# Kernel optimization log

Hardware: AMD Instinct MI355X
Metric: run time of the kernel (lower is better)

Reference implementation:

```python
import jax, jax.numpy as jnp
import numpy as np
from jax import lax

B, T, D, H = 32, 2048, 512, 512


def setup_inputs() -> dict:
    key = jax.random.key(0)
    k1, k2, k3 = jax.random.split(key, 3)
    inputs = jax.random.normal(k1, (B, T, D), dtype=jnp.float32)
    input_paddings = jnp.zeros((B, T), dtype=jnp.float32)  # all tokens valid
    c0 = jnp.zeros((B, H), dtype=jnp.float32)
    h0 = jnp.zeros((B, H), dtype=jnp.float32)
    # flax LSTMCell params fused: dense_i kernel [D,4H] (no bias), dense_h kernel [H,4H] + bias [4H]
    Wi = jax.random.normal(k2, (D, 4 * H), dtype=jnp.float32) * 0.05
    Wh = jax.random.normal(k3, (H, 4 * H), dtype=jnp.float32) * 0.05
    b = jnp.zeros((4 * H,), dtype=jnp.float32)
    return {"inputs": inputs, "input_paddings": input_paddings,
            "c0": c0, "h0": h0, "Wi": Wi, "Wh": Wh, "b": b}


def reference(inputs, input_paddings, c0, h0, Wi, Wh, b):
    # reverse=False path: lengths are computed but unused.
    del input_paddings
    # Precompute input projections for all timesteps in one big GEMM: [B,T,4H]
    x_proj = jnp.einsum('btd,dg->btg', inputs, Wi)

    def step(carry, xp_t):
        c, h = carry
        z = xp_t + h @ Wh + b  # [B, 4H]
        i, f, g, o = jnp.split(z, 4, axis=-1)  # flax gate order: i, f, g, o
        c_new = jax.nn.sigmoid(f) * c + jax.nn.sigmoid(i) * jnp.tanh(g)
        h_new = jax.nn.sigmoid(o) * jnp.tanh(c_new)
        return (c_new, h_new), h_new

    xs = jnp.swapaxes(x_proj, 0, 1)  # [T, B, 4H]
    _, outs = lax.scan(step, (c0, h0), xs)
    return jnp.swapaxes(outs, 0, 1)  # [B, T, H]
```

## Files before the change

### kernel.cpp

```cpp
#include <hip/hip_runtime.h>
#include <cstdint>
#include <cstddef>

#define TT 2048
#define DD 512

#define BM 128
#define BN 128
#define BK 16

__global__ __launch_bounds__(256) void xproj_gemm(
    const float* __restrict__ A,
    const float* __restrict__ W,
    const float* __restrict__ bias,
    float* __restrict__ C,
    int t0, int tmask, int tlog)
{
    __shared__ __align__(16) float As[BK][BM + 4];
    __shared__ __align__(16) float Bs[BK][BN + 4];
    const int tid = threadIdx.x;
    const int nt = blockIdx.x;
    const int mt = blockIdx.y;
    const int m_base = mt * BM;
    const int n_base = nt * BN;
    const int ty = tid >> 4;
    const int tx = tid & 15;

    float acc[8][8];
#pragma unroll
    for (int i = 0; i < 8; ++i)
#pragma unroll
        for (int j = 0; j < 8; ++j) acc[i][j] = 0.f;

    for (int k0 = 0; k0 < DD; k0 += BK) {
#pragma unroll
        for (int j = 0; j < 2; ++j) {
            int idx = tid * 2 + j;
            int rowl = idx >> 2, q = idx & 3;
            int rc = m_base + rowl;
            int rg = ((rc >> tlog) << 11) + t0 + (rc & tmask);
            float4 av = *(const float4*)(A + (size_t)rg * DD + k0 + q * 4);
            As[q * 4 + 0][rowl] = av.x;
            As[q * 4 + 1][rowl] = av.y;
            As[q * 4 + 2][rowl] = av.z;
            As[q * 4 + 3][rowl] = av.w;
            int kr = idx >> 5, nq = idx & 31;
            *(float4*)&Bs[kr][nq * 4] =
                *(const float4*)(W + (size_t)(k0 + kr) * 2048 + n_base + nq * 4);
        }
        __syncthreads();
#pragma unroll
        for (int kk = 0; kk < BK; ++kk) {
            float a[8], bb[8];
            *(float4*)&a[0]  = *(const float4*)&As[kk][ty * 8];
            *(float4*)&a[4]  = *(const float4*)&As[kk][ty * 8 + 4];
            *(float4*)&bb[0] = *(const float4*)&Bs[kk][tx * 8];
            *(float4*)&bb[4] = *(const float4*)&Bs[kk][tx * 8 + 4];
#pragma unroll
            for (int i = 0; i < 8; ++i)
#pragma unroll
                for (int j = 0; j < 8; ++j)
                    acc[i][j] = fmaf(a[i], bb[j], acc[i][j]);
        }
        __syncthreads();
    }
#pragma unroll
    for (int i = 0; i < 8; ++i) {
        int m = m_base + ty * 8 + i;
        int bglob = m >> tlog, tl = m & tmask;
#pragma unroll
        for (int j = 0; j < 8; j += 4) {
            int n = n_base + tx * 8 + j;
            int gate = n >> 9, c = n & 511;
            float4 v;
            v.x = acc[i][j + 0] + bias[n + 0];
            v.y = acc[i][j + 1] + bias[n + 1];
            v.z = acc[i][j + 2] + bias[n + 2];
            v.w = acc[i][j + 3] + bias[n + 3];
            size_t addr = (((size_t)tl * 4 + gate) * 32 + bglob) * 512 + c;
            *(float4*)(C + addr) = v;
        }
    }
}

#define NGRP 8
#define BPG  32
#define HSZ  (32 * 512)
#define POISON 0xFFFFFFFFu
#define WHST 516

__device__ __forceinline__ float ldg_agent_f32(const float* p) {
    return __hip_atomic_load(p, __ATOMIC_RELAXED, __HIP_MEMORY_SCOPE_AGENT);
}

template<int D, int HALF>
__device__ __forceinline__ void rstep(float* p, int lane) {
    const bool hi = (lane & D) != 0;
#pragma unroll
    for (int i = 0; i < HALF; ++i) {
        float send = hi ? p[i] : p[i + HALF];
        float recv = __shfl_xor(send, D, 64);
        p[i] = (hi ? p[i + HALF] : p[i]) + recv;
    }
}

__global__ __launch_bounds__(512) void lstm_scan(
    const float* __restrict__ xp,
    const float* __restrict__ Wh,
    const float* __restrict__ c0,
    const float* __restrict__ h0,
    float* __restrict__ out,
    float* hbuf,
    float* __restrict__ cbuf,
    int t0, int T_CH)
{
    __shared__ float wh[64 * WHST];
    __shared__ float hs[2 * 4 * 512];

    const int tid  = threadIdx.x;
    const int blk  = blockIdx.x;
    const int g    = blk >> 5;
    const int p    = blk & 31;
    const int j0   = p * 16;
    const int lane = tid & 63;
    const int w    = tid >> 6;

    const int idx = ((lane & 1) << 4) | ((lane & 2) << 2) | (lane & 4)
                  | ((lane >> 2) & 2) | ((lane >> 4) & 1);
    const int gate = idx >> 3;
    const int cc   = (idx >> 2) & 1;
    const int bq   = idx & 3;
    const int B    = 4 * g + bq;
    const int col  = j0 + 2 * w + cc;
    const bool low = lane < 32;
    const bool act = low && ((lane & 3) == 0);

    float creg = 0.f;
    if (act) {
        size_t o = (size_t)B * 512 + col;
        if (t0 == 0) {
            creg = c0[o];
            float hv = h0[o];
            if (__float_as_uint(hv) == POISON) hv = __uint_as_float(0xFFFFFFFEu);
            __hip_atomic_store(hbuf + o, hv, __ATOMIC_RELAXED, __HIP_MEMORY_SCOPE_AGENT);
        } else {
            creg = cbuf[o];
        }
    }

#pragma unroll
    for (int i = 0; i < 16; ++i) {
        int id = tid + i * 512;
        int q4 = id & 3, gt = (id >> 2) & 3, k = id >> 4;
        float4 v = *(const float4*)(Wh + (size_t)k * 2048 + gt * 512 + j0 + q4 * 4);
        int r0 = gt * 16 + q4 * 4;
        wh[(r0 + 0) * WHST + k] = v.x;
        wh[(r0 + 1) * WHST + k] = v.y;
        wh[(r0 + 2) * WHST + k] = v.z;
        wh[(r0 + 3) * WHST + k] = v.w;
    }

    const int sb = w >> 1;
    const int sh = (w & 1) * 256;

    float xr = 0.f, xn = 0.f;
    if (low) xr = xp[((size_t)gate * 32 + B) * 512 + col];

    __syncthreads();

    for (int tl = 0; tl < T_CH; ++tl) {
        const int t = t0 + tl;
        const int cur = t % 3;
        const int nxt = (t + 1) % 3;
        const int rcy = (t + 2) % 3;

        if (low && (tl + 1 < T_CH))
            xn = xp[((size_t)((tl + 1) * 4 + gate) * 32 + B) * 512 + col];

        const float* hsrc = hbuf + (size_t)cur * HSZ
                          + (size_t)(4 * g + sb) * 512 + sh + lane;
        float hvv[4];
        for (;;) {
            bool ok = true;
#pragma unroll
            for (int q = 0; q < 4; ++q) {
                hvv[q] = ldg_agent_f32(hsrc + q * 64);
                ok = ok & (__float_as_uint(hvv[q]) != POISON);
            }
            if (ok) break;
            __builtin_amdgcn_s_sleep(1);
        }
        float* hdst = hs + (tl & 1) * 2048 + sb * 512 + sh + lane;
#pragma unroll
        for (int q = 0; q < 4; ++q) hdst[q * 64] = hvv[q];
        __syncthreads();

        if (act)
            __hip_atomic_store(hbuf + (size_t)rcy * HSZ + (size_t)B * 512 + col,
                               __uint_as_float(POISON),
                               __ATOMIC_RELAXED, __HIP_MEMORY_SCOPE_AGENT);

        const float* hb = hs + (tl & 1) * 2048;
        float4 ha[4], h2[4];
#pragma unroll
        for (int b = 0; b < 4; ++b) {
            ha[b] = *(const float4*)(hb + b * 512 + 4 * lane);
            h2[b] = *(const float4*)(hb + b * 512 + 256 + 4 * lane);
        }
        float pp[32];
#pragma unroll
        for (int i = 0; i < 32; ++i) pp[i] = 0.f;
#pragma unroll
        for (int gt = 0; gt < 4; ++gt)
#pragma unroll
            for (int c2 = 0; c2 < 2; ++c2) {
                const float* wr = wh + (size_t)(gt * 16 + 2 * w + c2) * WHST + 4 * lane;
                float4 w0 = *(const float4*)wr;
                float4 w1 = *(const float4*)(wr + 256);
#pragma unroll
                for (int b = 0; b < 4; ++b) {
                    float a = pp[gt * 8 + c2 * 4 + b];
                    a = fmaf(ha[b].x, w0.x, a);
                    a = fmaf(ha[b].y, w0.y, a);
                    a = fmaf(ha[b].z, w0.z, a);
                    a = fmaf(ha[b].w, w0.w, a);
                    a = fmaf(h2[b].x, w1.x, a);
                    a = fmaf(h2[b].y, w1.y, a);
                    a = fmaf(h2[b].z, w1.z, a);
                    a = fmaf(h2[b].w, w1.w, a);
                    pp[gt * 8 + c2 * 4 + b] = a;
                }
            }

        rstep<1, 16>(pp, lane);
        rstep<2, 8>(pp, lane);
        rstep<4, 4>(pp, lane);
        rstep<8, 2>(pp, lane);
        rstep<16, 1>(pp, lane);
        float v0 = pp[0] + __shfl_xor(pp[0], 32, 64);

        float av = 0.f;
        if (low) {
            float zz = v0 + xr;
            av = (gate == 2) ? tanhf(zz) : 1.f / (1.f + expf(-zz));
        }
        float ag = __shfl_xor(av, 1, 64);
        float af = __shfl_xor(av, 2, 64);
        float ao = __shfl_xor(av, 3, 64);

        float hn = 0.f;
        if (act) {
            float cn = af * creg + av * ag;
            hn = ao * tanhf(cn);
            creg = cn;
        }
        asm volatile("s_waitcnt vmcnt(0)" ::: "memory");
        if (act) {
            __hip_atomic_store(hbuf + (size_t)nxt * HSZ + (size_t)B * 512 + col,
                               hn, __ATOMIC_RELAXED, __HIP_MEMORY_SCOPE_AGENT);
            out[((size_t)B * TT + t) * 512 + col] = hn;
        }
        if (low) xr = xn;
    }

    if (act) cbuf[(size_t)B * 512 + col] = creg;
}

extern "C" void kernel_launch(void* const* d_in, const int* in_sizes, int n_in,
                              void* d_out, int out_size, void* d_ws, size_t ws_size,
                              hipStream_t stream) {
    const float* inputs = (const float*)d_in[0];
    const float* c0   = (const float*)d_in[2];
    const float* h0   = (const float*)d_in[3];
    const float* Wi   = (const float*)d_in[4];
    const float* Wh   = (const float*)d_in[5];
    const float* bias = (const float*)d_in[6];
    float* out = (float*)d_out;

    float* ws_f = (float*)d_ws;
    float* hbuf = ws_f;
    float* cbuf = ws_f + 3 * HSZ;
    float* xp   = ws_f + 4 * HSZ;
    const size_t extras_bytes = (size_t)(4 * HSZ) * sizeof(float);

    int T_CH = 256;
    while (T_CH > 32 &&
           extras_bytes + (size_t)T_CH * 65536 * sizeof(float) > ws_size)
        T_CH >>= 1;
    int tlog = 31 - __builtin_clz((unsigned)T_CH);

    hipMemsetAsync(hbuf, 0xFF, (size_t)(3 * HSZ) * sizeof(float), stream);

    for (int t0 = 0; t0 < TT; t0 += T_CH) {
        dim3 g1(2048 / BN, (32 * T_CH) / BM);
        xproj_gemm<<<g1, 256, 0, stream>>>(inputs, Wi, bias, xp, t0, T_CH - 1, tlog);

        const float* xp_c = xp;
        int t0_arg = t0, tch_arg = T_CH;
        void* args[] = { (void*)&xp_c, (void*)&Wh, (void*)&c0, (void*)&h0,
                         (void*)&out, (void*)&hbuf, (void*)&cbuf,
                         (void*)&t0_arg, (void*)&tch_arg };
        hipLaunchCooperativeKernel((const void*)lstm_scan, dim3(NGRP * BPG), dim3(512),
                                   args, 0, stream);
    }
}
```

Before: 7.847 ms.

## Load h directly from global per wave, drop LDS staging and block barrier

Each wave now polls the full 4x512 hidden-state slice for its batch group straight from global memory with 64-bit agent-scope atomic loads, rather than cooperatively staging h into shared memory and calling __syncthreads. This removes the block-wide barrier and LDS round trip from the per-timestep critical path, so each wave proceeds as soon as its own data is ready. The cost is 8x redundant global/L2 traffic per block, since every wave reads the whole slice, and polling with many more outstanding loads per lane.

```diff
diff --git a/kernel.cpp b/kernel.cpp
--- a/kernel.cpp
+++ b/kernel.cpp
@@ -89,8 +89,10 @@
 #define POISON 0xFFFFFFFFu
 #define WHST 516
 
-__device__ __forceinline__ float ldg_agent_f32(const float* p) {
-    return __hip_atomic_load(p, __ATOMIC_RELAXED, __HIP_MEMORY_SCOPE_AGENT);
+__device__ __forceinline__ float2 ldg_agent_f2(const float* p) {
+    double d = __hip_atomic_load((const double*)p, __ATOMIC_RELAXED,
+                                 __HIP_MEMORY_SCOPE_AGENT);
+    return __builtin_bit_cast(float2, d);
 }
 
 template<int D, int HALF>
@@ -115,7 +117,6 @@
     int t0, int T_CH)
 {
     __shared__ float wh[64 * WHST];
-    __shared__ float hs[2 * 4 * 512];
 
     const int tid  = threadIdx.x;
     const int blk  = blockIdx.x;
@@ -160,9 +161,6 @@
         wh[(r0 + 3) * WHST + k] = v.w;
     }
 
-    const int sb = w >> 1;
-    const int sh = (w & 1) * 256;
-
     float xr = 0.f, xn = 0.f;
     if (low) xr = xp[((size_t)gate * 32 + B) * 512 + col];
 
@@ -177,36 +175,38 @@
         if (low && (tl + 1 < T_CH))
             xn = xp[((size_t)((tl + 1) * 4 + gate) * 32 + B) * 512 + col];
 
-        const float* hsrc = hbuf + (size_t)cur * HSZ
-                          + (size_t)(4 * g + sb) * 512 + sh + lane;
-        float hvv[4];
-        for (;;) {
-            bool ok = true;
-#pragma unroll
-            for (int q = 0; q < 4; ++q) {
-                hvv[q] = ldg_agent_f32(hsrc + q * 64);
-                ok = ok & (__float_as_uint(hvv[q]) != POISON);
+        float2 hlo[4][2], hhi[4][2];
+        {
+            const float* hb = hbuf + (size_t)cur * HSZ
+                            + (size_t)(4 * g) * 512 + 4 * lane;
+            for (;;) {
+                bool ok = true;
+#pragma unroll
+                for (int b = 0; b < 4; ++b) {
+                    const float* pb = hb + b * 512;
+                    hlo[b][0] = ldg_agent_f2(pb);
+                    hlo[b][1] = ldg_agent_f2(pb + 2);
+                    hhi[b][0] = ldg_agent_f2(pb + 256);
+                    hhi[b][1] = ldg_agent_f2(pb + 258);
+#pragma unroll
+                    for (int q = 0; q < 2; ++q) {
+                        ok = ok & (__float_as_uint(hlo[b][q].x) != POISON)
+                               & (__float_as_uint(hlo[b][q].y) != POISON)
+                               & (__float_as_uint(hhi[b][q].x) != POISON)
+                               & (__float_as_uint(hhi[b][q].y) != POISON);
+                    }
+                }
+                if (__all(ok)) break;
+                __builtin_amdgcn_s_sleep(1);
             }
-            if (ok) break;
-            __builtin_amdgcn_s_sleep(1);
-        }
-        float* hdst = hs + (tl & 1) * 2048 + sb * 512 + sh + lane;
-#pragma unroll
-        for (int q = 0; q < 4; ++q) hdst[q * 64] = hvv[q];
-        __syncthreads();
+        }
+        __builtin_amdgcn_sched_barrier(0);
 
         if (act)
             __hip_atomic_store(hbuf + (size_t)rcy * HSZ + (size_t)B * 512 + col,
                                __uint_as_float(POISON),
                                __ATOMIC_RELAXED, __HIP_MEMORY_SCOPE_AGENT);
 
-        const float* hb = hs + (tl & 1) * 2048;
-        float4 ha[4], h2[4];
-#pragma unroll
-        for (int b = 0; b < 4; ++b) {
-            ha[b] = *(const float4*)(hb + b * 512 + 4 * lane);
-            h2[b] = *(const float4*)(hb + b * 512 + 256 + 4 * lane);
-        }
         float pp[32];
 #pragma unroll
         for (int i = 0; i < 32; ++i) pp[i] = 0.f;
@@ -220,14 +220,14 @@
 #pragma unroll
                 for (int b = 0; b < 4; ++b) {
                     float a = pp[gt * 8 + c2 * 4 + b];
-                    a = fmaf(ha[b].x, w0.x, a);
-                    a = fmaf(ha[b].y, w0.y, a);
-                    a = fmaf(ha[b].z, w0.z, a);
-                    a = fmaf(ha[b].w, w0.w, a);
-                    a = fmaf(h2[b].x, w1.x, a);
-                    a = fmaf(h2[b].y, w1.y, a);
-                    a = fmaf(h2[b].z, w1.z, a);
-                    a = fmaf(h2[b].w, w1.w, a);
+                    a = fmaf(hlo[b][0].x, w0.x, a);
+                    a = fmaf(hlo[b][0].y, w0.y, a);
+                    a = fmaf(hlo[b][1].x, w0.z, a);
+                    a = fmaf(hlo[b][1].y, w0.w, a);
+                    a = fmaf(hhi[b][0].x, w1.x, a);
+                    a = fmaf(hhi[b][0].y, w1.y, a);
+                    a = fmaf(hhi[b][1].x, w1.z, a);
+                    a = fmaf(hhi[b][1].y, w1.w, a);
                     pp[gt * 8 + c2 * 4 + b] = a;
                 }
             }
```

Measured after the change: 29.91 ms. 3.81x slower.

## Overlap next chunk's input-projection GEMM with LSTM scan via extra warps

Applied to the files above, without the earlier changes.

Fuses the input-projection GEMM for the next time chunk into the cooperative LSTM scan kernel. Four extra wavefronts per block compute it into a double-buffered workspace while the original eight wavefronts run the recurrence. This hides the separate GEMM launches behind the latency-bound scan. Because the two warp groups now share a block, __syncthreads is replaced by LDS counter-based soft barriers and the recurrence section runs at raised wave priority. The risks are contention for CU resources and memory bandwidth, which could slow the critical recurrence path, and higher register pressure from the 768-thread launch bound.

```diff
diff --git a/kernel.cpp b/kernel.cpp
--- a/kernel.cpp
+++ b/kernel.cpp
@@ -93,6 +93,13 @@
     return __hip_atomic_load(p, __ATOMIC_RELAXED, __HIP_MEMORY_SCOPE_AGENT);
 }
 
+__device__ __forceinline__ void soft_bar(unsigned* ctr, bool leader, unsigned target) {
+    asm volatile("s_waitcnt lgkmcnt(0)" ::: "memory");
+    if (leader)
+        __hip_atomic_fetch_add(ctr, 1u, __ATOMIC_RELAXED, __HIP_MEMORY_SCOPE_WORKGROUP);
+    while (__hip_atomic_load(ctr, __ATOMIC_RELAXED, __HIP_MEMORY_SCOPE_WORKGROUP) < target) {}
+}
+
 template<int D, int HALF>
 __device__ __forceinline__ void rstep(float* p, int lane) {
     const bool hi = (lane & D) != 0;
@@ -104,18 +111,25 @@
     }
 }
 
-__global__ __launch_bounds__(512) void lstm_scan(
+__global__ __launch_bounds__(768) void lstm_fused(
     const float* __restrict__ xp,
+    const float* __restrict__ A,
+    const float* __restrict__ Wi,
+    const float* __restrict__ bias,
+    float* __restrict__ xpn,
     const float* __restrict__ Wh,
     const float* __restrict__ c0,
     const float* __restrict__ h0,
     float* __restrict__ out,
     float* hbuf,
     float* __restrict__ cbuf,
-    int t0, int T_CH)
+    int t0, int T_CH, int ngt, int tlog2)
 {
     __shared__ float wh[64 * WHST];
     __shared__ float hs[2 * 4 * 512];
+    __shared__ __align__(16) float As2[16][68];
+    __shared__ __align__(16) float Bs2[16][68];
+    __shared__ unsigned scnt, gcnt;
 
     const int tid  = threadIdx.x;
     const int blk  = blockIdx.x;
@@ -125,145 +139,233 @@
     const int lane = tid & 63;
     const int w    = tid >> 6;
 
-    const int idx = ((lane & 1) << 4) | ((lane & 2) << 2) | (lane & 4)
-                  | ((lane >> 2) & 2) | ((lane >> 4) & 1);
-    const int gate = idx >> 3;
-    const int cc   = (idx >> 2) & 1;
-    const int bq   = idx & 3;
-    const int B    = 4 * g + bq;
-    const int col  = j0 + 2 * w + cc;
-    const bool low = lane < 32;
-    const bool act = low && ((lane & 3) == 0);
-
-    float creg = 0.f;
-    if (act) {
-        size_t o = (size_t)B * 512 + col;
-        if (t0 == 0) {
-            creg = c0[o];
-            float hv = h0[o];
-            if (__float_as_uint(hv) == POISON) hv = __uint_as_float(0xFFFFFFFEu);
-            __hip_atomic_store(hbuf + o, hv, __ATOMIC_RELAXED, __HIP_MEMORY_SCOPE_AGENT);
-        } else {
-            creg = cbuf[o];
-        }
-    }
-
-#pragma unroll
-    for (int i = 0; i < 16; ++i) {
-        int id = tid + i * 512;
-        int q4 = id & 3, gt = (id >> 2) & 3, k = id >> 4;
-        float4 v = *(const float4*)(Wh + (size_t)k * 2048 + gt * 512 + j0 + q4 * 4);
-        int r0 = gt * 16 + q4 * 4;
-        wh[(r0 + 0) * WHST + k] = v.x;
-        wh[(r0 + 1) * WHST + k] = v.y;
-        wh[(r0 + 2) * WHST + k] = v.z;
-        wh[(r0 + 3) * WHST + k] = v.w;
-    }
-
-    const int sb = w >> 1;
-    const int sh = (w & 1) * 256;
-
-    float xr = 0.f, xn = 0.f;
-    if (low) xr = xp[((size_t)gate * 32 + B) * 512 + col];
+    if (tid == 0) { scnt = 0u; gcnt = 0u; }
+
+    int gate = 0, cc = 0, B = 0, col = 0;
+    bool low = false, act = false;
+    float creg = 0.f, xr = 0.f, xn = 0.f;
+    if (tid < 512) {
+        const int idx = ((lane & 1) << 4) | ((lane & 2) << 2) | (lane & 4)
+                      | ((lane >> 2) & 2) | ((lane >> 4) & 1);
+        gate = idx >> 3;
+        cc   = (idx >> 2) & 1;
+        const int bq = idx & 3;
+        B    = 4 * g + bq;
+        col  = j0 + 2 * w + cc;
+        low  = lane < 32;
+        act  = low && ((lane & 3) == 0);
+
+        if (act) {
+            size_t o = (size_t)B * 512 + col;
+            if (t0 == 0) {
+                creg = c0[o];
+                float hv = h0[o];
+                if (__float_as_uint(hv) == POISON) hv = __uint_as_float(0xFFFFFFFEu);
+                __hip_atomic_store(hbuf + o, hv, __ATOMIC_RELAXED, __HIP_MEMORY_SCOPE_AGENT);
+            } else {
+                creg = cbuf[o];
+            }
+        }
+
+#pragma unroll
+        for (int i = 0; i < 16; ++i) {
+            int id = tid + i * 512;
+            int q4 = id & 3, gt = (id >> 2) & 3, k = id >> 4;
+            float4 v = *(const float4*)(Wh + (size_t)k * 2048 + gt * 512 + j0 + q4 * 4);
+            int r0 = gt * 16 + q4 * 4;
+            wh[(r0 + 0) * WHST + k] = v.x;
+            wh[(r0 + 1) * WHST + k] = v.y;
+            wh[(r0 + 2) * WHST + k] = v.z;
+            wh[(r0 + 3) * WHST + k] = v.w;
+        }
+        if (low) xr = xp[((size_t)gate * 32 + B) * 512 + col];
+    }
 
     __syncthreads();
 
-    for (int tl = 0; tl < T_CH; ++tl) {
-        const int t = t0 + tl;
-        const int cur = t % 3;
-        const int nxt = (t + 1) % 3;
-        const int rcy = (t + 2) % 3;
-
-        if (low && (tl + 1 < T_CH))
-            xn = xp[((size_t)((tl + 1) * 4 + gate) * 32 + B) * 512 + col];
-
-        const float* hsrc = hbuf + (size_t)cur * HSZ
-                          + (size_t)(4 * g + sb) * 512 + sh + lane;
-        float hvv[4];
-        for (;;) {
-            bool ok = true;
-#pragma unroll
-            for (int q = 0; q < 4; ++q) {
-                hvv[q] = ldg_agent_f32(hsrc + q * 64);
-                ok = ok & (__float_as_uint(hvv[q]) != POISON);
-            }
-            if (ok) break;
-            __builtin_amdgcn_s_sleep(1);
-        }
-        float* hdst = hs + (tl & 1) * 2048 + sb * 512 + sh + lane;
-#pragma unroll
-        for (int q = 0; q < 4; ++q) hdst[q * 64] = hvv[q];
-        __syncthreads();
-
-        if (act)
-            __hip_atomic_store(hbuf + (size_t)rcy * HSZ + (size_t)B * 512 + col,
-                               __uint_as_float(POISON),
-                               __ATOMIC_RELAXED, __HIP_MEMORY_SCOPE_AGENT);
-
-        const float* hb = hs + (tl & 1) * 2048;
-        float4 ha[4], h2[4];
-#pragma unroll
-        for (int b = 0; b < 4; ++b) {
-            ha[b] = *(const float4*)(hb + b * 512 + 4 * lane);
-            h2[b] = *(const float4*)(hb + b * 512 + 256 + 4 * lane);
-        }
-        float pp[32];
-#pragma unroll
-        for (int i = 0; i < 32; ++i) pp[i] = 0.f;
-#pragma unroll
-        for (int gt = 0; gt < 4; ++gt)
-#pragma unroll
-            for (int c2 = 0; c2 < 2; ++c2) {
-                const float* wr = wh + (size_t)(gt * 16 + 2 * w + c2) * WHST + 4 * lane;
-                float4 w0 = *(const float4*)wr;
-                float4 w1 = *(const float4*)(wr + 256);
-#pragma unroll
-                for (int b = 0; b < 4; ++b) {
-                    float a = pp[gt * 8 + c2 * 4 + b];
-                    a = fmaf(ha[b].x, w0.x, a);
-                    a = fmaf(ha[b].y, w0.y, a);
-                    a = fmaf(ha[b].z, w0.z, a);
-                    a = fmaf(ha[b].w, w0.w, a);
-                    a = fmaf(h2[b].x, w1.x, a);
-                    a = fmaf(h2[b].y, w1.y, a);
-                    a = fmaf(h2[b].z, w1.z, a);
-                    a = fmaf(h2[b].w, w1.w, a);
-                    pp[gt * 8 + c2 * 4 + b] = a;
+    if (tid < 512) {
+        const int sb = w >> 1;
+        const int sh = (w & 1) * 256;
+        unsigned starget = 0;
+
+        for (int tl = 0; tl < T_CH; ++tl) {
+            const int t = t0 + tl;
+            const int cur = t % 3;
+            const int nxt = (t + 1) % 3;
+            const int rcy = (t + 2) % 3;
+
+            if (low && (tl + 1 < T_CH))
+                xn = xp[((size_t)((tl + 1) * 4 + gate) * 32 + B) * 512 + col];
+
+            const float* hsrc = hbuf + (size_t)cur * HSZ
+                              + (size_t)(4 * g + sb) * 512 + sh + lane;
+            float hvv[4];
+            for (;;) {
+                bool ok = true;
+#pragma unroll
+                for (int q = 0; q < 4; ++q) {
+                    hvv[q] = ldg_agent_f32(hsrc + q * 64);
+                    ok = ok & (__float_as_uint(hvv[q]) != POISON);
                 }
-            }
-
-        rstep<1, 16>(pp, lane);
-        rstep<2, 8>(pp, lane);
-        rstep<4, 4>(pp, lane);
-        rstep<8, 2>(pp, lane);
-        rstep<16, 1>(pp, lane);
-        float v0 = pp[0] + __shfl_xor(pp[0], 32, 64);
-
-        float av = 0.f;
-        if (low) {
-            float zz = v0 + xr;
-            av = (gate == 2) ? tanhf(zz) : 1.f / (1.f + expf(-zz));
-        }
-        float ag = __shfl_xor(av, 1, 64);
-        float af = __shfl_xor(av, 2, 64);
-        float ao = __shfl_xor(av, 3, 64);
-
-        float hn = 0.f;
-        if (act) {
-            float cn = af * creg + av * ag;
-            hn = ao * tanhf(cn);
-            creg = cn;
-        }
-        asm volatile("s_waitcnt vmcnt(0)" ::: "memory");
-        if (act) {
-            __hip_atomic_store(hbuf + (size_t)nxt * HSZ + (size_t)B * 512 + col,
-                               hn, __ATOMIC_RELAXED, __HIP_MEMORY_SCOPE_AGENT);
-            out[((size_t)B * TT + t) * 512 + col] = hn;
-        }
-        if (low) xr = xn;
-    }
-
-    if (act) cbuf[(size_t)B * 512 + col] = creg;
+                if (ok) break;
+                __builtin_amdgcn_s_sleep(1);
+            }
+            float* hdst = hs + (tl & 1) * 2048 + sb * 512 + sh + lane;
+#pragma unroll
+            for (int q = 0; q < 4; ++q) hdst[q * 64] = hvv[q];
+
+            starget += 8;
+            soft_bar(&scnt, lane == 0, starget);
+
+            if (act)
+                __hip_atomic_store(hbuf + (size_t)rcy * HSZ + (size_t)B * 512 + col,
+                                   __uint_as_float(POISON),
+                                   __ATOMIC_RELAXED, __HIP_MEMORY_SCOPE_AGENT);
+
+            __builtin_amdgcn_s_setprio(1);
+            const float* hb = hs + (tl & 1) * 2048;
+            float4 ha[4], h2[4];
+#pragma unroll
+            for (int b = 0; b < 4; ++b) {
+                ha[b] = *(const float4*)(hb + b * 512 + 4 * lane);
+                h2[b] = *(const float4*)(hb + b * 512 + 256 + 4 * lane);
+            }
+            float pp[32];
+#pragma unroll
+            for (int i = 0; i < 32; ++i) pp[i] = 0.f;
+#pragma unroll
+            for (int gt = 0; gt < 4; ++gt)
+#pragma unroll
+                for (int c2 = 0; c2 < 2; ++c2) {
+                    const float* wr = wh + (size_t)(gt * 16 + 2 * w + c2) * WHST + 4 * lane;
+                    float4 w0 = *(const float4*)wr;
+                    float4 w1 = *(const float4*)(wr + 256);
+#pragma unroll
+                    for (int b = 0; b < 4; ++b) {
+                        float a = pp[gt * 8 + c2 * 4 + b];
+                        a = fmaf(ha[b].x, w0.x, a);
+                        a = fmaf(ha[b].y, w0.y, a);
+                        a = fmaf(ha[b].z, w0.z, a);
+                        a = fmaf(ha[b].w, w0.w, a);
+                        a = fmaf(h2[b].x, w1.x, a);
+                        a = fmaf(h2[b].y, w1.y, a);
+                        a = fmaf(h2[b].z, w1.z, a);
+                        a = fmaf(h2[b].w, w1.w, a);
+                        pp[gt * 8 + c2 * 4 + b] = a;
+                    }
+                }
+
+            rstep<1, 16>(pp, lane);
+            rstep<2, 8>(pp, lane);
+            rstep<4, 4>(pp, lane);
+            rstep<8, 2>(pp, lane);
+            rstep<16, 1>(pp, lane);
+            float v0 = pp[0] + __shfl_xor(pp[0], 32, 64);
+
+            float av = 0.f;
+            if (low) {
+                float zz = v0 + xr;
+                av = (gate == 2) ? tanhf(zz) : 1.f / (1.f + expf(-zz));
+            }
+            float ag = __shfl_xor(av, 1, 64);
+            float af = __shfl_xor(av, 2, 64);
+            float ao = __shfl_xor(av, 3, 64);
+            __builtin_amdgcn_s_setprio(0);
+
+            float hn = 0.f;
+            if (act) {
+                float cn = af * creg + av * ag;
+                hn = ao * tanhf(cn);
+                creg = cn;
+            }
+            asm volatile("s_waitcnt vmcnt(0)" ::: "memory");
+            if (act) {
+                __hip_atomic_store(hbuf + (size_t)nxt * HSZ + (size_t)B * 512 + col,
+                                   hn, __ATOMIC_RELAXED, __HIP_MEMORY_SCOPE_AGENT);
+                out[((size_t)B * TT + t) * 512 + col] = hn;
+            }
+            if (low) xr = xn;
+        }
+
+        if (act) cbuf[(size_t)B * 512 + col] = creg;
+
+    } else if (ngt > 0) {
+        const int id  = tid - 512;
+        const int ty2 = id >> 4, tx2 = id & 15;
+        const int tmask2 = T_CH - 1;
+        const int t0n = t0 + T_CH;
+        unsigned gtarget = 0;
+
+        for (int tile = 0; tile < ngt; ++tile) {
+            int tt  = blk * ngt + tile;
+            int mt2 = tt >> 5, nt2 = tt & 31;
+
+            int am = id >> 2, akq = id & 3;
+            int arc = mt2 * 64 + am;
+            int abg = arc >> tlog2, atl = arc & tmask2;
+            const float* arow = A + (size_t)(abg * 2048 + t0n + atl) * DD;
+            int bkr = id >> 4, bnq = id & 15;
+
+            float acc2[4][4];
+#pragma unroll
+            for (int i = 0; i < 4; ++i)
+#pragma unroll
+                for (int j = 0; j < 4; ++j) acc2[i][j] = 0.f;
+
+            for (int k0 = 0; k0 < DD; k0 += 16) {
+                float4 av = *(const float4*)(arow + k0 + 4 * akq);
+                float4 bv = *(const float4*)(Wi + (size_t)(k0 + bkr) * 2048
+                                             + nt2 * 64 + 4 * bnq);
+                As2[akq * 4 + 0][am] = av.x;
+                As2[akq * 4 + 1][am] = av.y;
+                As2[akq * 4 + 2][am] = av.z;
+                As2[akq * 4 + 3][am] = av.w;
+                *(float4*)&Bs2[bkr][bnq * 4] = bv;
+
+                gtarget += 4;
+                soft_bar(&gcnt, lane == 0, gtarget);
+#pragma unroll
+                for (int kk = 0; kk < 16; ++kk) {
+                    float4 a4 = *(const float4*)&As2[kk][ty2 * 4];
+                    float4 b4 = *(const float4*)&Bs2[kk][tx2 * 4];
+                    acc2[0][0] = fmaf(a4.x, b4.x, acc2[0][0]);
+                    acc2[0][1] = fmaf(a4.x, b4.y, acc2[0][1]);
+                    acc2[0][2] = fmaf(a4.x, b4.z, acc2[0][2]);
+                    acc2[0][3] = fmaf(a4.x, b4.w, acc2[0][3]);
+                    acc2[1][0] = fmaf(a4.y, b4.x, acc2[1][0]);
+                    acc2[1][1] = fmaf(a4.y, b4.y, acc2[1][1]);
+                    acc2[1][2] = fmaf(a4.y, b4.z, acc2[1][2]);
+                    acc2[1][3] = fmaf(a4.y, b4.w, acc2[1][3]);
+                    acc2[2][0] = fmaf(a4.z, b4.x, acc2[2][0]);
+                    acc2[2][1] = fmaf(a4.z, b4.y, acc2[2][1]);
+                    acc2[2][2] = fmaf(a4.z, b4.z, acc2[2][2]);
+                    acc2[2][3] = fmaf(a4.z, b4.w, acc2[2][3]);
+                    acc2[3][0] = fmaf(a4.w, b4.x, acc2[3][0]);
+                    acc2[3][1] = fmaf(a4.w, b4.y, acc2[3][1]);
+                    acc2[3][2] = fmaf(a4.w, b4.z, acc2[3][2]);
+                    acc2[3][3] = fmaf(a4.w, b4.w, acc2[3][3]);
+                }
+                gtarget += 4;
+                soft_bar(&gcnt, lane == 0, gtarget);
+            }
+
+            int nb = nt2 * 64 + tx2 * 4;
+            int gt2 = nb >> 9, c512 = nb & 511;
+            float4 bsv = *(const float4*)(bias + nb);
+#pragma unroll
+            for (int i = 0; i < 4; ++i) {
+                int rc = mt2 * 64 + ty2 * 4 + i;
+                int bg = rc >> tlog2, tl2 = rc & tmask2;
+                float4 v;
+                v.x = acc2[i][0] + bsv.x;
+                v.y = acc2[i][1] + bsv.y;
+                v.z = acc2[i][2] + bsv.z;
+                v.w = acc2[i][3] + bsv.w;
+                size_t addr = (((size_t)tl2 * 4 + gt2) * 32 + bg) * 512 + c512;
+                *(float4*)(xpn + addr) = v;
+            }
+        }
+    }
 }
 
 extern "C" void kernel_launch(void* const* d_in, const int* in_sizes, int n_in,
@@ -280,27 +382,49 @@
     float* ws_f = (float*)d_ws;
     float* hbuf = ws_f;
     float* cbuf = ws_f + 3 * HSZ;
-    float* xp   = ws_f + 4 * HSZ;
-    const size_t extras_bytes = (size_t)(4 * HSZ) * sizeof(float);
-
-    int T_CH = 256;
-    while (T_CH > 32 &&
-           extras_bytes + (size_t)T_CH * 65536 * sizeof(float) > ws_size)
-        T_CH >>= 1;
-    int tlog = 31 - __builtin_clz((unsigned)T_CH);
+    float* xpA  = ws_f + 4 * HSZ;
+
+    int T_CH = 0;
+    int dbuf = 1;
+    for (int tc = 256; tc >= 32; tc >>= 1) {
+        if ((size_t)(4 * HSZ + 2 * (size_t)tc * 65536) * sizeof(float) <= ws_size) {
+            T_CH = tc; break;
+        }
+    }
+    if (T_CH == 0) {
+        dbuf = 0;
+        T_CH = 256;
+        while (T_CH > 32 &&
+               (size_t)(4 * HSZ + (size_t)T_CH * 65536) * sizeof(float) > ws_size)
+            T_CH >>= 1;
+    }
+    const int tlog = 31 - __builtin_clz((unsigned)T_CH);
+    float* xpB = dbuf ? (xpA + (size_t)T_CH * 65536) : xpA;
+    const int nch = TT / T_CH;
 
     hipMemsetAsync(hbuf, 0xFF, (size_t)(3 * HSZ) * sizeof(float), stream);
 
-    for (int t0 = 0; t0 < TT; t0 += T_CH) {
-        dim3 g1(2048 / BN, (32 * T_CH) / BM);
-        xproj_gemm<<<g1, 256, 0, stream>>>(inputs, Wi, bias, xp, t0, T_CH - 1, tlog);
-
-        const float* xp_c = xp;
-        int t0_arg = t0, tch_arg = T_CH;
-        void* args[] = { (void*)&xp_c, (void*)&Wh, (void*)&c0, (void*)&h0,
+    dim3 g1(2048 / BN, (32 * T_CH) / BM);
+    xproj_gemm<<<g1, 256, 0, stream>>>(inputs, Wi, bias, xpA, 0, T_CH - 1, tlog);
+
+    for (int n = 0; n < nch; ++n) {
+        float* cur = (n & 1) ? xpB : xpA;
+        float* nxt = ((n + 1) & 1) ? xpB : xpA;
+        int ngt = (dbuf && (n + 1 < nch)) ? (T_CH / 16) : 0;
+
+        if (!dbuf && n > 0)
+            xproj_gemm<<<g1, 256, 0, stream>>>(inputs, Wi, bias, xpA,
+                                               n * T_CH, T_CH - 1, tlog);
+
+        const float* cur_c = cur;
+        float* nxt_m = nxt;
+        int t0_arg = n * T_CH, tch_arg = T_CH, ngt_arg = ngt, tlog_arg = tlog;
+        void* args[] = { (void*)&cur_c, (void*)&inputs, (void*)&Wi, (void*)&bias,
+                         (void*)&nxt_m, (void*)&Wh, (void*)&c0, (void*)&h0,
                          (void*)&out, (void*)&hbuf, (void*)&cbuf,
-                         (void*)&t0_arg, (void*)&tch_arg };
-        hipLaunchCooperativeKernel((const void*)lstm_scan, dim3(NGRP * BPG), dim3(512),
-                                   args, 0, stream);
-    }
-}
+                         (void*)&t0_arg, (void*)&tch_arg, (void*)&ngt_arg,
+                         (void*)&tlog_arg };
+        hipLaunchCooperativeKernel((const void*)lstm_fused, dim3(NGRP * BPG),
+                                   dim3(768), args, 0, stream);
+    }
+}
```

New measurement: 8.309 ms. 5.9% more time.

## Replace per-step block barrier with LDS counter barrier and use DPP lane swaps

Applied to the files above, without the earlier changes.

Replaces the __syncthreads in the recurrent LSTM step with a software barrier: each wave's leader increments a shared-memory counter and all waves spin until it reaches the running target. It also swaps the xor-1/xor-2/xor-3 lane shuffles (in the reduction and the gate exchange) for DPP quad permutes, and drops the explicit vmcnt(0) wait before publishing h. The aim is to cut per-timestep latency on the serial critical path. The risks are memory-ordering problems: LDS writes of h may not be visible across waves, and removing the vmcnt wait can let the new h be published before the poison store to the recycled slot completes.

```diff
diff --git a/kernel.cpp b/kernel.cpp
--- a/kernel.cpp
+++ b/kernel.cpp
@@ -93,13 +93,31 @@
     return __hip_atomic_load(p, __ATOMIC_RELAXED, __HIP_MEMORY_SCOPE_AGENT);
 }
 
+template<int CTRL>
+__device__ __forceinline__ float dppf(float x) {
+    return __int_as_float(
+        __builtin_amdgcn_update_dpp(0, __float_as_int(x), CTRL, 0xf, 0xf, true));
+}
+
+__device__ __forceinline__ void soft_bar(unsigned* ctr, bool leader, unsigned target) {
+    asm volatile("s_waitcnt lgkmcnt(0)" ::: "memory");
+    if (leader)
+        __hip_atomic_fetch_add(ctr, 1u, __ATOMIC_RELAXED, __HIP_MEMORY_SCOPE_WORKGROUP);
+    while (__hip_atomic_load(ctr, __ATOMIC_RELAXED, __HIP_MEMORY_SCOPE_WORKGROUP) < target)
+        __builtin_amdgcn_s_sleep(1);
+    __builtin_amdgcn_sched_barrier(0);
+}
+
 template<int D, int HALF>
 __device__ __forceinline__ void rstep(float* p, int lane) {
     const bool hi = (lane & D) != 0;
 #pragma unroll
     for (int i = 0; i < HALF; ++i) {
         float send = hi ? p[i] : p[i + HALF];
-        float recv = __shfl_xor(send, D, 64);
+        float recv;
+        if constexpr (D == 1)      recv = dppf<0xB1>(send);
+        else if constexpr (D == 2) recv = dppf<0x4E>(send);
+        else                       recv = __shfl_xor(send, D, 64);
         p[i] = (hi ? p[i + HALF] : p[i]) + recv;
     }
 }
@@ -116,6 +134,7 @@
 {
     __shared__ float wh[64 * WHST];
     __shared__ float hs[2 * 4 * 512];
+    __shared__ unsigned scnt;
 
     const int tid  = threadIdx.x;
     const int blk  = blockIdx.x;
@@ -134,6 +153,8 @@
     const int col  = j0 + 2 * w + cc;
     const bool low = lane < 32;
     const bool act = low && ((lane & 3) == 0);
+
+    if (tid == 0) scnt = 0u;
 
     float creg = 0.f;
     if (act) {
@@ -168,6 +189,8 @@
 
     __syncthreads();
 
+    unsigned starget = 0;
+
     for (int tl = 0; tl < T_CH; ++tl) {
         const int t = t0 + tl;
         const int cur = t % 3;
@@ -193,12 +216,15 @@
         float* hdst = hs + (tl & 1) * 2048 + sb * 512 + sh + lane;
 #pragma unroll
         for (int q = 0; q < 4; ++q) hdst[q * 64] = hvv[q];
-        __syncthreads();
+
+        starget += 8;
+        soft_bar(&scnt, lane == 0, starget);
 
         if (act)
             __hip_atomic_store(hbuf + (size_t)rcy * HSZ + (size_t)B * 512 + col,
                                __uint_as_float(POISON),
                                __ATOMIC_RELAXED, __HIP_MEMORY_SCOPE_AGENT);
+        asm volatile("" ::: "memory");
 
         const float* hb = hs + (tl & 1) * 2048;
         float4 ha[4], h2[4];
@@ -244,18 +270,15 @@
             float zz = v0 + xr;
             av = (gate == 2) ? tanhf(zz) : 1.f / (1.f + expf(-zz));
         }
-        float ag = __shfl_xor(av, 1, 64);
-        float af = __shfl_xor(av, 2, 64);
-        float ao = __shfl_xor(av, 3, 64);
+        float ag = dppf<0xB1>(av);
+        float af = dppf<0x4E>(av);
+        float ao = dppf<0x1B>(av);
 
         float hn = 0.f;
         if (act) {
             float cn = af * creg + av * ag;
             hn = ao * tanhf(cn);
             creg = cn;
-        }
-        asm volatile("s_waitcnt vmcnt(0)" ::: "memory");
-        if (act) {
             __hip_atomic_store(hbuf + (size_t)nxt * HSZ + (size_t)B * 512 + col,
                                hn, __ATOMIC_RELAXED, __HIP_MEMORY_SCOPE_AGENT);
             out[((size_t)B * TT + t) * 512 + col] = hn;
```

New measurement: 7.721 ms. About the same (-1.6%).
